# Kernel optimization log

Measured on AMD Instinct MI355X. Metric: run time of the kernel, lower is better.

## Reference

```python
import jax, jax.numpy as jnp
import numpy as np
import math

B, N, D_MODEL, D_QK, D_V = 8, 2048, 512, 64, 64
NEG_INF = float('-inf')

def setup_inputs() -> dict:
    key = jax.random.key(0)
    k1, k2, k3, k4, k5 = jax.random.split(key, 5)
    mask = jax.random.randint(k1, (B, N, N), 0, 2).astype(bool)
    x_key_value = jax.random.normal(k2, (B, N, D_MODEL), dtype=jnp.float32)
    wk = jax.random.normal(k3, (D_MODEL, D_QK), dtype=jnp.float32) * 0.02
    wq = jax.random.normal(k4, (D_MODEL, D_QK), dtype=jnp.float32) * 0.02
    wv = jax.random.normal(k5, (D_MODEL, D_V), dtype=jnp.float32) * 0.02
    return {"mask": mask, "x_key_value": x_key_value, "wk": wk, "wq": wq, "wv": wv}

def reference(mask, x_key_value, wk, wq, wv):
    # self-attention: x_query defaults to x_key_value
    div = math.sqrt(wk.shape[1])
    k = x_key_value @ wk          # [n, j, d_qk]
    q = x_key_value @ wq          # [n, i, d_qk]
    v = x_key_value @ wv          # [n, j, d_v]
    mat = jnp.einsum('nik,njk->nij', q, k) / div
    mat = jnp.where(mask, mat, NEG_INF)
    portion = jax.nn.softmax(mat, axis=2)
    return jnp.einsum('nij,njk->nik', portion, v)
```

## Files before the change

kernel.cpp:

```cpp
#include <hip/hip_runtime.h>
#include <hip/hip_bf16.h>

typedef __attribute__((ext_vector_type(8))) short bf16x8;
typedef __attribute__((ext_vector_type(4))) float f32x4;
typedef __hip_bfloat16 bf16;

#define BATCH 8
#define SEQ   2048
#define DMODEL 512
#define DHEAD 64
#define ROWS (BATCH * SEQ)
#define LOG2E 1.44269504f

#define PROJ_BLOCKS (ROWS / 32)
#define PACK_BLOCKS 1024

static __device__ inline short f2bf(float f) {
    union { __hip_bfloat16 h; short s; } u;
    u.h = __float2bfloat16(f);
    return u.s;
}

__global__ __launch_bounds__(256) void transpose_w_kernel(
    const float* __restrict__ wq, const float* __restrict__ wk,
    const float* __restrict__ wv, bf16* __restrict__ wt)
{
    const int s  = blockIdx.x / 8;
    const int kt = blockIdx.x % 8;
    const float* w = (s == 0) ? wq : ((s == 1) ? wk : wv);

    __shared__ float Ts[64][68];

    const int tid = threadIdx.x;
    int nr = tid >> 4;
    int n4 = (tid & 15) * 4;
#pragma unroll
    for (int p = 0; p < 4; ++p) {
        int k = 16 * p + nr;
        float4 v = *(const float4*)(w + (size_t)(kt * 64 + k) * DHEAD + n4);
        Ts[k][n4] = v.x; Ts[k][n4 + 1] = v.y; Ts[k][n4 + 2] = v.z; Ts[k][n4 + 3] = v.w;
    }
    __syncthreads();
#pragma unroll
    for (int p = 0; p < 2; ++p) {
        int cc = tid + p * 256;
        int n = cc >> 3;
        int kk = (cc & 7) * 8;
        bf16x8 o;
#pragma unroll
        for (int e = 0; e < 8; ++e) o[e] = f2bf(Ts[kk + e][n]);
        *(bf16x8*)(wt + (size_t)(s * 64 + n) * DMODEL + kt * 64 + kk) = o;
    }
}

__global__ __launch_bounds__(512) void proj_pack_kernel(
    const float* __restrict__ x, const bf16* __restrict__ wt,
    const int* __restrict__ mask,
    bf16* __restrict__ Q, bf16* __restrict__ K, bf16* __restrict__ Vt,
    unsigned long long* __restrict__ mb)
{
    if (blockIdx.x >= PROJ_BLOCKS) {
        const int wvid = (blockIdx.x - PROJ_BLOCKS) * 8 + (threadIdx.x >> 6);
        const int lane = threadIdx.x & 63;
        const int* mp = mask + (size_t)wvid * 4096 + lane;
        unsigned long long word = 0;
#pragma unroll 8
        for (int w = 0; w < 64; ++w) {
            int v = mp[(size_t)w * 64];
            unsigned long long bal = __ballot(v != 0);
            if (lane == w) word = bal;
        }
        mb[(size_t)wvid * 64 + lane] = word;
        return;
    }

    const int r0 = blockIdx.x * 32;
    const int tid = threadIdx.x;
    const int lane = tid & 63;
    const int wid = tid >> 6;
    const int strip = wid & 1;
    const int cq = wid >> 1;
    const int l15 = lane & 15;
    const int quad = lane >> 4;

    f32x4 acc[3] = {};

    const float* xp = x + (size_t)(r0 + 16 * strip + l15) * DMODEL;

    for (int k0 = 0; k0 < DMODEL; k0 += 64) {
        float4 xa = *(const float4*)(xp + k0 + quad * 8);
        float4 xb = *(const float4*)(xp + k0 + quad * 8 + 4);
        float4 xc = *(const float4*)(xp + k0 + 32 + quad * 8);
        float4 xd = *(const float4*)(xp + k0 + 32 + quad * 8 + 4);
        bf16x8 a0, a1;
        a0[0] = f2bf(xa.x); a0[1] = f2bf(xa.y); a0[2] = f2bf(xa.z); a0[3] = f2bf(xa.w);
        a0[4] = f2bf(xb.x); a0[5] = f2bf(xb.y); a0[6] = f2bf(xb.z); a0[7] = f2bf(xb.w);
        a1[0] = f2bf(xc.x); a1[1] = f2bf(xc.y); a1[2] = f2bf(xc.z); a1[3] = f2bf(xc.w);
        a1[4] = f2bf(xd.x); a1[5] = f2bf(xd.y); a1[6] = f2bf(xd.z); a1[7] = f2bf(xd.w);
#pragma unroll
        for (int g = 0; g < 3; ++g) {
            int n = 16 * (3 * cq + g) + l15;
            const bf16* wp = wt + (size_t)n * DMODEL + k0 + quad * 8;
            bf16x8 b0 = *(const bf16x8*)(wp);
            bf16x8 b1 = *(const bf16x8*)(wp + 32);
            acc[g] = __builtin_amdgcn_mfma_f32_16x16x32_bf16(a0, b0, acc[g], 0, 0, 0);
            acc[g] = __builtin_amdgcn_mfma_f32_16x16x32_bf16(a1, b1, acc[g], 0, 0, 0);
        }
    }

#pragma unroll
    for (int g = 0; g < 3; ++g) {
        int ng = 16 * (3 * cq + g) + l15;
        int sel = ng >> 6;
        int col = ng & 63;
#pragma unroll
        for (int r = 0; r < 4; ++r) {
            int row = r0 + 16 * strip + quad * 4 + r;
            union { __hip_bfloat16 h; bf16 b; } u;
            u.h = __float2bfloat16(acc[g][r]);
            if (sel == 0)      Q[(size_t)row * DHEAD + col] = u.b;
            else if (sel == 1) K[(size_t)row * DHEAD + col] = u.b;
            else {
                int bb = row >> 11, j = row & (SEQ - 1);
                Vt[((size_t)bb * DHEAD + col) * SEQ + j] = u.b;
            }
        }
    }
}

__global__ __launch_bounds__(256) void flash_kernel(
    const bf16* __restrict__ Q, const bf16* __restrict__ K,
    const bf16* __restrict__ Vt, const unsigned long long* __restrict__ mb,
    float* __restrict__ out)
{
    const int b = blockIdx.y;
    const int q0 = blockIdx.x * 16;
    const int tid = threadIdx.x;
    const int lane = tid & 63;
    const int wid = tid >> 6;
    const int l15 = lane & 15;
    const int quad = lane >> 4;

    __shared__ __align__(16) bf16 Ps[4][16][72];
    __shared__ float Om[4][16][64];
    __shared__ float Mw[4][16];
    __shared__ float Lw[4][16];

    const bf16* qp = Q + ((size_t)(b * SEQ + q0 + l15)) * DHEAD + quad * 8;
    bf16x8 aQ0 = *(const bf16x8*)(qp);
    bf16x8 aQ1 = *(const bf16x8*)(qp + 32);

    f32x4 oacc[4] = {};
    float m_i[4], l_i[4];
#pragma unroll
    for (int r = 0; r < 4; ++r) { m_i[r] = -1e30f; l_i[r] = 0.f; }

    const unsigned long long* mrow = mb + ((size_t)(b * SEQ + q0 + quad * 4)) * 32;
    const int jbase = wid * (SEQ / 4);

    for (int jt = 0; jt < SEQ / 4; jt += 64) {
        const int j0 = jbase + jt;

        unsigned long long mrw[4];
#pragma unroll
        for (int r = 0; r < 4; ++r) mrw[r] = mrow[(size_t)r * 32 + (j0 >> 6)];

        f32x4 sacc[4] = {};
#pragma unroll
        for (int c = 0; c < 4; ++c) {
            const bf16* kp = K + ((size_t)(b * SEQ + j0 + 16 * c + l15)) * DHEAD + quad * 8;
            bf16x8 b0 = *(const bf16x8*)(kp);
            bf16x8 b1 = *(const bf16x8*)(kp + 32);
            sacc[c] = __builtin_amdgcn_mfma_f32_16x16x32_bf16(aQ0, b0, sacc[c], 0, 0, 0);
            sacc[c] = __builtin_amdgcn_mfma_f32_16x16x32_bf16(aQ1, b1, sacc[c], 0, 0, 0);
        }

#pragma unroll
        for (int r = 0; r < 4; ++r) {
            unsigned long long mr = mrw[r] >> l15;
            unsigned m0 = (unsigned)mr;
            unsigned m1 = (unsigned)(mr >> 32);
            sacc[0][r] = (m0 & 1u)         ? sacc[0][r] * 0.125f : -1e30f;
            sacc[1][r] = ((m0 >> 16) & 1u) ? sacc[1][r] * 0.125f : -1e30f;
            sacc[2][r] = (m1 & 1u)         ? sacc[2][r] * 0.125f : -1e30f;
            sacc[3][r] = ((m1 >> 16) & 1u) ? sacc[3][r] * 0.125f : -1e30f;
        }

#pragma unroll
        for (int r = 0; r < 4; ++r) {
            float rm = fmaxf(fmaxf(sacc[0][r], sacc[1][r]), fmaxf(sacc[2][r], sacc[3][r]));
            rm = fmaxf(rm, __shfl_xor(rm, 1));
            rm = fmaxf(rm, __shfl_xor(rm, 2));
            rm = fmaxf(rm, __shfl_xor(rm, 4));
            rm = fmaxf(rm, __shfl_xor(rm, 8));
            float mn = fmaxf(m_i[r], rm);
            float alpha = exp2f((m_i[r] - mn) * LOG2E);
            m_i[r] = mn;
            float rs = 0.f;
#pragma unroll
            for (int c = 0; c < 4; ++c) {
                float pv = exp2f((sacc[c][r] - mn) * LOG2E);
                sacc[c][r] = pv;
                rs += pv;
            }
            rs += __shfl_xor(rs, 1);
            rs += __shfl_xor(rs, 2);
            rs += __shfl_xor(rs, 4);
            rs += __shfl_xor(rs, 8);
            l_i[r] = l_i[r] * alpha + rs;
#pragma unroll
            for (int c = 0; c < 4; ++c) oacc[c][r] *= alpha;
        }

#pragma unroll
        for (int c = 0; c < 4; ++c)
#pragma unroll
            for (int r = 0; r < 4; ++r) {
                union { __hip_bfloat16 h; bf16 b; } u;
                u.h = __float2bfloat16(sacc[c][r]);
                Ps[wid][quad * 4 + r][16 * c + l15] = u.b;
            }

        bf16x8 aP0 = *(const bf16x8*)(&Ps[wid][l15][quad * 8]);
        bf16x8 aP1 = *(const bf16x8*)(&Ps[wid][l15][32 + quad * 8]);
#pragma unroll
        for (int c = 0; c < 4; ++c) {
            const bf16* vp = Vt + ((size_t)b * DHEAD + 16 * c + l15) * SEQ + j0 + quad * 8;
            bf16x8 v0 = *(const bf16x8*)(vp);
            bf16x8 v1 = *(const bf16x8*)(vp + 32);
            oacc[c] = __builtin_amdgcn_mfma_f32_16x16x32_bf16(aP0, v0, oacc[c], 0, 0, 0);
            oacc[c] = __builtin_amdgcn_mfma_f32_16x16x32_bf16(aP1, v1, oacc[c], 0, 0, 0);
        }
    }

#pragma unroll
    for (int c = 0; c < 4; ++c)
#pragma unroll
        for (int r = 0; r < 4; ++r)
            Om[wid][quad * 4 + r][16 * c + l15] = oacc[c][r];
    if (l15 == 0) {
#pragma unroll
        for (int r = 0; r < 4; ++r) {
            Mw[wid][quad * 4 + r] = m_i[r];
            Lw[wid][quad * 4 + r] = l_i[r];
        }
    }
    __syncthreads();

    {
        int row = tid >> 4;
        int c0 = (tid & 15) * 4;
        float M = fmaxf(fmaxf(Mw[0][row], Mw[1][row]), fmaxf(Mw[2][row], Mw[3][row]));
        float sc0 = exp2f((Mw[0][row] - M) * LOG2E);
        float sc1 = exp2f((Mw[1][row] - M) * LOG2E);
        float sc2 = exp2f((Mw[2][row] - M) * LOG2E);
        float sc3 = exp2f((Mw[3][row] - M) * LOG2E);
        float L = Lw[0][row] * sc0 + Lw[1][row] * sc1 + Lw[2][row] * sc2 + Lw[3][row] * sc3;
        float invL = 1.0f / L;
        float4 o;
        float* op = (float*)&o;
#pragma unroll
        for (int e = 0; e < 4; ++e) {
            op[e] = (Om[0][row][c0 + e] * sc0 + Om[1][row][c0 + e] * sc1 +
                     Om[2][row][c0 + e] * sc2 + Om[3][row][c0 + e] * sc3) * invL;
        }
        *(float4*)(out + ((size_t)(b * SEQ + q0 + row)) * DHEAD + c0) = o;
    }
}

extern "C" void kernel_launch(void* const* d_in, const int* in_sizes, int n_in,
                              void* d_out, int out_size, void* d_ws, size_t ws_size,
                              hipStream_t stream)
{
    const int*   mask = (const int*)d_in[0];
    const float* x    = (const float*)d_in[1];
    const float* wk   = (const float*)d_in[2];
    const float* wq   = (const float*)d_in[3];
    const float* wv   = (const float*)d_in[4];
    float* out = (float*)d_out;

    bf16* Qb = (bf16*)d_ws;
    bf16* Kb = Qb + (size_t)ROWS * DHEAD;
    bf16* Vt = Kb + (size_t)ROWS * DHEAD;
    bf16* Wt = Vt + (size_t)BATCH * DHEAD * SEQ;
    unsigned long long* Mb = (unsigned long long*)(Wt + 3 * (size_t)DHEAD * DMODEL);

    transpose_w_kernel<<<dim3(24), 256, 0, stream>>>(wq, wk, wv, Wt);
    proj_pack_kernel<<<dim3(PROJ_BLOCKS + PACK_BLOCKS), 512, 0, stream>>>(
        x, Wt, mask, Qb, Kb, Vt, Mb);
    flash_kernel<<<dim3(SEQ / 16, BATCH), 256, 0, stream>>>(Qb, Kb, Vt, Mb, out);
}
```

Measured before the change: 310.0 us.

## Pack mask with vectorized int4 loads and interleaved bit layout

Each lane of the mask-packing path now loads an int4, covering four consecutive mask entries, and issues four ballots per load instead of one strided scalar load per ballot. The packed bitmask therefore uses a new interleaved layout: each group of 256 columns is stored as four 64-bit words, with word k holding columns where index mod 4 equals k. The attention kernel's mask lookup and bit-extraction shifts are rewritten to match. The goal is coalesced, wider reads of the large mask tensor. The cost is a more complex indexing scheme that producer and consumer must keep in agreement.

```diff
diff --git a/kernel.cpp b/kernel.cpp
--- a/kernel.cpp
+++ b/kernel.cpp
@@ -14,6 +14,9 @@
 
 #define PROJ_BLOCKS (ROWS / 32)
 #define PACK_BLOCKS 1024
+#define PACK_NT (PACK_BLOCKS * 512)
+#define TOT4 (BATCH * SEQ * SEQ / 4)
+#define PACK_ITERS (TOT4 / PACK_NT)
 
 static __device__ inline short f2bf(float f) {
     union { __hip_bfloat16 h; short s; } u;
@@ -60,17 +63,27 @@
     unsigned long long* __restrict__ mb)
 {
     if (blockIdx.x >= PROJ_BLOCKS) {
-        const int wvid = (blockIdx.x - PROJ_BLOCKS) * 8 + (threadIdx.x >> 6);
-        const int lane = threadIdx.x & 63;
-        const int* mp = mask + (size_t)wvid * 4096 + lane;
-        unsigned long long word = 0;
-#pragma unroll 8
-        for (int w = 0; w < 64; ++w) {
-            int v = mp[(size_t)w * 64];
-            unsigned long long bal = __ballot(v != 0);
-            if (lane == w) word = bal;
-        }
-        mb[(size_t)wvid * 64 + lane] = word;
+        const int pb = blockIdx.x - PROJ_BLOCKS;
+        const int tid = threadIdx.x;
+        const int lane = tid & 63;
+        const int g = pb * 512 + tid;
+        const int wv = g >> 6;
+#pragma unroll 4
+        for (int it = 0; it < PACK_ITERS; ++it) {
+            size_t idx4 = (size_t)g + (size_t)it * PACK_NT;
+            int4 v = ((const int4*)mask)[idx4];
+            unsigned long long B0 = __ballot(v.x != 0);
+            unsigned long long B1 = __ballot(v.y != 0);
+            unsigned long long B2 = __ballot(v.z != 0);
+            unsigned long long B3 = __ballot(v.w != 0);
+            if (lane < 4) {
+                unsigned long long s01 = (lane & 1) ? B1 : B0;
+                unsigned long long s23 = (lane & 1) ? B3 : B2;
+                unsigned long long wd  = (lane & 2) ? s23 : s01;
+                size_t W = (size_t)wv + (size_t)it * (PACK_NT >> 6);
+                mb[4 * W + lane] = wd;
+            }
+        }
         return;
     }
 
@@ -155,15 +168,17 @@
 #pragma unroll
     for (int r = 0; r < 4; ++r) { m_i[r] = -1e30f; l_i[r] = 0.f; }
 
-    const unsigned long long* mrow = mb + ((size_t)(b * SEQ + q0 + quad * 4)) * 32;
     const int jbase = wid * (SEQ / 4);
-
-    for (int jt = 0; jt < SEQ / 4; jt += 64) {
-        const int j0 = jbase + jt;
+    const unsigned long long* mq =
+        mb + (((size_t)(b * SEQ + q0 + quad * 4)) * 8 + wid * 2) * 4 + (l15 & 3);
+    const int shl = l15 >> 2;
+
+    for (int kk = 0; kk < 8; ++kk) {
+        const int j0 = jbase + kk * 64;
 
         unsigned long long mrw[4];
 #pragma unroll
-        for (int r = 0; r < 4; ++r) mrw[r] = mrow[(size_t)r * 32 + (j0 >> 6)];
+        for (int r = 0; r < 4; ++r) mrw[r] = mq[(size_t)r * 32 + (kk >> 2) * 4];
 
         f32x4 sacc[4] = {};
 #pragma unroll
@@ -175,15 +190,14 @@
             sacc[c] = __builtin_amdgcn_mfma_f32_16x16x32_bf16(aQ1, b1, sacc[c], 0, 0, 0);
         }
 
+        const int sh = (kk & 3) * 16 + shl;
 #pragma unroll
         for (int r = 0; r < 4; ++r) {
-            unsigned long long mr = mrw[r] >> l15;
-            unsigned m0 = (unsigned)mr;
-            unsigned m1 = (unsigned)(mr >> 32);
-            sacc[0][r] = (m0 & 1u)         ? sacc[0][r] * 0.125f : -1e30f;
-            sacc[1][r] = ((m0 >> 16) & 1u) ? sacc[1][r] * 0.125f : -1e30f;
-            sacc[2][r] = (m1 & 1u)         ? sacc[2][r] * 0.125f : -1e30f;
-            sacc[3][r] = ((m1 >> 16) & 1u) ? sacc[3][r] * 0.125f : -1e30f;
+            unsigned m = (unsigned)(mrw[r] >> sh);
+            sacc[0][r] = (m & 1u)         ? sacc[0][r] * 0.125f : -1e30f;
+            sacc[1][r] = ((m >> 4) & 1u)  ? sacc[1][r] * 0.125f : -1e30f;
+            sacc[2][r] = ((m >> 8) & 1u)  ? sacc[2][r] * 0.125f : -1e30f;
+            sacc[3][r] = ((m >> 12) & 1u) ? sacc[3][r] * 0.125f : -1e30f;
         }
 
 #pragma unroll
```

Result: no change. 309.7 us (-0.1%).
